# Optimization experiments

Measured on AMD Instinct MI355X. Metric: run time of the kernel, lower is better.

## Reference

```python
import jax, jax.numpy as jnp
import numpy as np

Z, DIM_IN, DIM_TS, DIM_OUT = 4096, 256, 2048, 256


def setup_inputs() -> dict:
    key = jax.random.key(0)
    k1, k2, k3 = jax.random.split(key, 3)
    features = jax.random.normal(k1, (Z, DIM_IN), dtype=jnp.float32)
    # Dense stand-in for the sparse CG buffer T: [dim_ts, dim_in * dim_in]
    T = jax.random.normal(k2, (DIM_TS, DIM_IN * DIM_IN), dtype=jnp.float32) * 0.02
    # KernelLinear output (learned mixing weights): [dim_out, dim_ts]
    W = jax.random.normal(k3, (DIM_OUT, DIM_TS), dtype=jnp.float32) * 0.02
    return {"features": features, "T": T, "W": W}


def reference(features, T, W):
    # features: [..., dim_in]; flatten leading dims as in the torch module
    *size, n = features.shape
    x = features.reshape(-1, n)                       # [z, i]
    # (T.t() @ W.T).T == W @ T ; reshape to [k, i, j]
    K = (W @ T).reshape(W.shape[0], n, n)             # [k, i, j]
    # per-sample bilinear (quadratic) form
    out = jnp.einsum('kij,zi,zj->zk', K, x, x)        # [z, k]
    return out.reshape(*size, -1)
```

## Files before the change

kernel.cpp:

```cpp
#include <hip/hip_runtime.h>

#define ZDIM 4096
#define DIN  256
#define DTS  2048
#define DOUT 256
#define CDIM 65536
#define SPLIT 16
#define NJS  8
#define NI   16
#define NST  (NJS * NI)
#define ZP   256
#define TILE_B 16384

typedef float fv4 __attribute__((ext_vector_type(4)));
typedef __bf16 bv8 __attribute__((ext_vector_type(8)));
typedef unsigned short u16;
typedef u16 uv8 __attribute__((ext_vector_type(8)));
typedef u16 uv4 __attribute__((ext_vector_type(4)));

union BC  { __bf16 b; u16 u; };
union VC8 { uv8 u; bv8 b; };
union FU  { unsigned u; float f; };

static __device__ __forceinline__ u16  f2b(float f){ BC c; c.b=(__bf16)f; return c.u; }
static __device__ __forceinline__ float bu(u16 v){ FU c; c.u = ((unsigned)v) << 16; return c.f; }
static __device__ __forceinline__ bv8  asb(uv8 x){ VC8 c; c.u=x; return c.b; }
static __device__ __forceinline__ uv8  pack8(fv4 a, fv4 b){
  uv8 p;
  p[0]=f2b(a[0]); p[1]=f2b(a[1]); p[2]=f2b(a[2]); p[3]=f2b(a[3]);
  p[4]=f2b(b[0]); p[5]=f2b(b[1]); p[6]=f2b(b[2]); p[7]=f2b(b[3]);
  return p;
}


__global__ __launch_bounds__(512, 2) void k_wt(const float* __restrict__ W,
                                               const float* __restrict__ T,
                                               u16* __restrict__ Km) {
  __shared__ u16 Al[256 * 40];
  __shared__ u16 Bl[32 * 128];
  const int tid  = threadIdx.x;
  const int lane = tid & 63;
  const int wave = tid >> 6;
  const int wk = (wave >> 1) * 64;
  const int wc = (wave & 1) * 64;
  const int cb = blockIdx.x * 128;
  const int ar = lane & 15, tg = lane >> 4;

  fv4 acc[4][4];
#pragma unroll
  for (int m = 0; m < 4; ++m)
#pragma unroll
    for (int n = 0; n < 4; ++n)
#pragma unroll
      for (int r = 0; r < 4; ++r) acc[m][n][r] = 0.f;

  for (int t0 = 0; t0 < DTS; t0 += 32) {
#pragma unroll
    for (int p = 0; p < 2; ++p) {
      int oct = tid + p * 512;
      int kr = oct >> 2, ts = (oct & 3) * 8;
      const float* src = W + (size_t)kr * DTS + t0 + ts;
      fv4 a = *(const fv4*)src, b = *(const fv4*)(src + 4);
      *(uv8*)&Al[kr * 40 + ts] = pack8(a, b);
    }
    {
      int tr = tid >> 4, co = (tid & 15) * 8;
      const float* src = T + (size_t)(t0 + tr) * CDIM + cb + co;
      fv4 a = *(const fv4*)src, b = *(const fv4*)(src + 4);
      *(uv8*)&Bl[tr * 128 + co] = pack8(a, b);
    }
    __syncthreads();
    bv8 af[4];
#pragma unroll
    for (int m = 0; m < 4; ++m)
      af[m] = asb(*(const uv8*)&Al[(wk + m * 16 + ar) * 40 + tg * 8]);
#pragma unroll
    for (int n = 0; n < 4; ++n) {
      uv8 bu2;
#pragma unroll
      for (int e = 0; e < 8; ++e)
        bu2[e] = Bl[(tg * 8 + e) * 128 + wc + n * 16 + ar];
      bv8 bf = asb(bu2);
#pragma unroll
      for (int m = 0; m < 4; ++m)
        acc[m][n] = __builtin_amdgcn_mfma_f32_16x16x32_bf16(af[m], bf, acc[m][n], 0, 0, 0);
    }
    __syncthreads();
  }
  const int ig = cb >> 8;
  const int j0 = cb & 255;
#pragma unroll
  for (int m = 0; m < 4; ++m)
#pragma unroll
    for (int n = 0; n < 4; ++n) {
      int j  = j0 + wc + n * 16;
      int js = j >> 5;
      int jj = j & 31;
      int sc = ig >> 4, il = ig & 15;
      size_t tb = ((size_t)(sc * 128 + js * 16 + il)) * TILE_B;
#pragma unroll
      for (int r = 0; r < 4; ++r) {
        int kr = wk + m * 16 + tg * 4 + r;
        int e  = kr * 64 + (jj + ar) * 2;
        e ^= ((e >> 7) & 7) << 4;
        *(u16*)((char*)Km + tb + e) = f2b(acc[m][n][r]);
      }
    }
}

__global__ __launch_bounds__(1024) void k_bil(const float* __restrict__ X,
                                              const u16* __restrict__ Km,
                                              u16* __restrict__ P) {
  __shared__ u16 Kl[2][TILE_B / 2];
  __shared__ u16 Xb[256 * 40];
  __shared__ u16 Xt[256 * 16];
  const int tid  = threadIdx.x;
  const int lane = tid & 63;
  const int wave = tid >> 6;
  const int wz   = (wave >> 2) * 64;
  const int wk   = (wave & 3) * 64;
  const int bid  = blockIdx.x;
  const int s    = bid & 15;
  const int z0   = (bid >> 4) * ZP;
  const int i0   = s * NI;
  const int ar   = lane & 15, tg = lane >> 4;

  const char* chunk = (const char*)Km + (size_t)s * NST * TILE_B;

  {
    int z = tid >> 2, ip = (tid & 3) * 4;
    fv4 v = *(const fv4*)&X[(size_t)(z0 + z) * DIN + i0 + ip];
    uv4 o;
#pragma unroll
    for (int e = 0; e < 4; ++e) o[e] = f2b(v[e]);
    *(uv4*)&Xt[z * 16 + ip] = o;
  }
  __builtin_amdgcn_global_load_lds(
      (const __attribute__((address_space(1))) void*)(chunk + (size_t)tid * 16),
      (__attribute__((address_space(3))) void*)((char*)&Kl[0][0] + tid * 16),
      16, 0, 0);

  int boff[4], aoff[4], xoff[4];
#pragma unroll
  for (int n = 0; n < 4; ++n) {
    int k = wk + n * 16 + ar;
    int e = k * 64 + tg * 16;
    boff[n] = e ^ (((e >> 7) & 7) << 4);
  }
#pragma unroll
  for (int m = 0; m < 4; ++m) {
    aoff[m] = (wz + m * 16 + ar) * 40 + tg * 8;
    xoff[m] = (wz + m * 16 + ar) * 16;
  }

  fv4 acc[4][4];
#pragma unroll
  for (int m = 0; m < 4; ++m)
#pragma unroll
    for (int n = 0; n < 4; ++n)
#pragma unroll
      for (int r = 0; r < 4; ++r) acc[m][n][r] = 0.f;

  for (int js = 0; js < NJS; ++js) {
    {
      int z = tid >> 2, seg = (tid & 3) * 8;
      const float* src = &X[(size_t)(z0 + z) * DIN + js * 32 + seg];
      fv4 a = *(const fv4*)src, b = *(const fv4*)(src + 4);
      *(uv8*)&Xb[z * 40 + seg] = pack8(a, b);
    }
    __syncthreads();

    uv8 af[4];
#pragma unroll
    for (int m = 0; m < 4; ++m)
      af[m] = *(const uv8*)&Xb[aoff[m]];

    for (int i = 0; i < NI; ++i) {
      const int st = js * NI + i;
      if (st + 1 < NST)
        __builtin_amdgcn_global_load_lds(
            (const __attribute__((address_space(1))) void*)(chunk + (size_t)(st + 1) * TILE_B + (size_t)tid * 16),
            (__attribute__((address_space(3))) void*)((char*)&Kl[(st + 1) & 1][0] + tid * 16),
            16, 0, 0);
      float xi[4];
#pragma unroll
      for (int m = 0; m < 4; ++m) xi[m] = bu(Xt[xoff[m] + i]);
      const char* kb = (const char*)&Kl[st & 1][0];
      bv8 bf[4];
#pragma unroll
      for (int n = 0; n < 4; ++n)
        bf[n] = asb(*(const uv8*)(kb + boff[n]));
#pragma unroll
      for (int m = 0; m < 4; ++m) {
        uv8 ap;
#pragma unroll
        for (int e = 0; e < 8; ++e) ap[e] = f2b(xi[m] * bu(af[m][e]));
        bv8 apb = asb(ap);
#pragma unroll
        for (int n = 0; n < 4; ++n)
          acc[m][n] = __builtin_amdgcn_mfma_f32_16x16x32_bf16(apb, bf[n], acc[m][n], 0, 0, 0);
      }
      __syncthreads();
    }
  }

  u16* dst = P + (size_t)s * (ZDIM * DOUT) + (size_t)z0 * DOUT;
#pragma unroll
  for (int m = 0; m < 4; ++m)
#pragma unroll
    for (int n = 0; n < 4; ++n)
#pragma unroll
      for (int r = 0; r < 4; ++r)
        dst[(size_t)(wz + m * 16 + tg * 4 + r) * DOUT + wk + n * 16 + ar] =
            f2b(acc[m][n][r]);
}

__global__ __launch_bounds__(256) void k_red(const u16* __restrict__ P,
                                             float* __restrict__ O) {
  size_t idx = ((size_t)blockIdx.x * 256 + threadIdx.x) * 4;
  fv4 acc;
#pragma unroll
  for (int r = 0; r < 4; ++r) acc[r] = 0.f;
#pragma unroll
  for (int p = 0; p < SPLIT; ++p) {
    uv4 v = *(const uv4*)&P[(size_t)p * (ZDIM * DOUT) + idx];
#pragma unroll
    for (int r = 0; r < 4; ++r) acc[r] += bu(v[r]);
  }
  *(fv4*)&O[idx] = acc;
}

extern "C" void kernel_launch(void* const* d_in, const int* in_sizes, int n_in,
                              void* d_out, int out_size, void* d_ws, size_t ws_size,
                              hipStream_t stream) {
  const float* feat = (const float*)d_in[0];
  const float* T    = (const float*)d_in[1];
  const float* W    = (const float*)d_in[2];
  float* out = (float*)d_out;

  u16* Km = (u16*)d_ws;
  u16* P  = (u16*)((char*)d_ws + (size_t)DOUT * CDIM * 2);

  k_wt <<<dim3(512),  dim3(512),  0, stream>>>(W, T, Km);
  k_bil<<<dim3(256),  dim3(1024), 0, stream>>>(feat, Km, P);
  k_red<<<dim3(1024), dim3(256),  0, stream>>>(P, out);
}
```

Measured before the change: 342.7 us.

## Triple-buffer K tiles and register-stage operands in both GEMM kernels

In k_bil, K tiles move from a double buffer to a triple buffer with a prefetch depth of two. The full __syncthreads is replaced by s_waitcnt vmcnt(1) plus a raw barrier, and the inner loop is unrolled with a macro. X operand fragments now load straight from global memory into registers instead of going through an LDS staging buffer, and the per-iteration xi scalars come from vectors preloaded once. In k_wt, W fragments load directly from global memory instead of LDS, T tiles are double-buffered with register prefetch and a padded stride, and the occupancy hint is raised to 4 blocks per SM. This aims to hide global-load latency and remove barriers and LDS traffic, but it adds redundant global W/X reads per wave and relies on hand-tuned vmcnt accounting that must match the order in which loads are issued.

```diff
diff --git a/kernel.cpp b/kernel.cpp
--- a/kernel.cpp
+++ b/kernel.cpp
@@ -33,11 +33,10 @@
 }
 
 
-__global__ __launch_bounds__(512, 2) void k_wt(const float* __restrict__ W,
+__global__ __launch_bounds__(512, 4) void k_wt(const float* __restrict__ W,
                                                const float* __restrict__ T,
                                                u16* __restrict__ Km) {
-  __shared__ u16 Al[256 * 40];
-  __shared__ u16 Bl[32 * 128];
+  __shared__ u16 Bl[2][32 * 130];
   const int tid  = threadIdx.x;
   const int lane = tid & 63;
   const int wave = tid >> 6;
@@ -45,6 +44,13 @@
   const int wc = (wave & 1) * 64;
   const int cb = blockIdx.x * 128;
   const int ar = lane & 15, tg = lane >> 4;
+  const int tr = tid >> 4, co = (tid & 15) * 8;
+
+  {
+    const float* src = T + (size_t)tr * CDIM + cb + co;
+    *(uv8*)&Bl[0][tr * 130 + co] = pack8(*(const fv4*)src, *(const fv4*)(src + 4));
+  }
+  __syncthreads();
 
   fv4 acc[4][4];
 #pragma unroll
@@ -54,38 +60,35 @@
 #pragma unroll
       for (int r = 0; r < 4; ++r) acc[m][n][r] = 0.f;
 
+  int buf = 0;
   for (int t0 = 0; t0 < DTS; t0 += 32) {
-#pragma unroll
-    for (int p = 0; p < 2; ++p) {
-      int oct = tid + p * 512;
-      int kr = oct >> 2, ts = (oct & 3) * 8;
-      const float* src = W + (size_t)kr * DTS + t0 + ts;
-      fv4 a = *(const fv4*)src, b = *(const fv4*)(src + 4);
-      *(uv8*)&Al[kr * 40 + ts] = pack8(a, b);
-    }
-    {
-      int tr = tid >> 4, co = (tid & 15) * 8;
-      const float* src = T + (size_t)(t0 + tr) * CDIM + cb + co;
-      fv4 a = *(const fv4*)src, b = *(const fv4*)(src + 4);
-      *(uv8*)&Bl[tr * 128 + co] = pack8(a, b);
-    }
-    __syncthreads();
+    const bool stg = (t0 + 32 < DTS);
+    fv4 ta, tb;
+    if (stg) {
+      const float* src = T + (size_t)(t0 + 32 + tr) * CDIM + cb + co;
+      ta = *(const fv4*)src; tb = *(const fv4*)(src + 4);
+    }
     bv8 af[4];
 #pragma unroll
-    for (int m = 0; m < 4; ++m)
-      af[m] = asb(*(const uv8*)&Al[(wk + m * 16 + ar) * 40 + tg * 8]);
+    for (int m = 0; m < 4; ++m) {
+      const float* wsrc = W + (size_t)(wk + m * 16 + ar) * DTS + t0 + tg * 8;
+      af[m] = asb(pack8(*(const fv4*)wsrc, *(const fv4*)(wsrc + 4)));
+    }
 #pragma unroll
     for (int n = 0; n < 4; ++n) {
       uv8 bu2;
 #pragma unroll
       for (int e = 0; e < 8; ++e)
-        bu2[e] = Bl[(tg * 8 + e) * 128 + wc + n * 16 + ar];
+        bu2[e] = Bl[buf][(tg * 8 + e) * 130 + wc + n * 16 + ar];
       bv8 bf = asb(bu2);
 #pragma unroll
       for (int m = 0; m < 4; ++m)
         acc[m][n] = __builtin_amdgcn_mfma_f32_16x16x32_bf16(af[m], bf, acc[m][n], 0, 0, 0);
     }
+    if (stg)
+      *(uv8*)&Bl[buf ^ 1][tr * 130 + co] = pack8(ta, tb);
     __syncthreads();
+    buf ^= 1;
   }
   const int ig = cb >> 8;
   const int j0 = cb & 255;
@@ -97,13 +100,13 @@
       int js = j >> 5;
       int jj = j & 31;
       int sc = ig >> 4, il = ig & 15;
-      size_t tb = ((size_t)(sc * 128 + js * 16 + il)) * TILE_B;
+      size_t tb2 = ((size_t)(sc * 128 + js * 16 + il)) * TILE_B;
 #pragma unroll
       for (int r = 0; r < 4; ++r) {
         int kr = wk + m * 16 + tg * 4 + r;
         int e  = kr * 64 + (jj + ar) * 2;
         e ^= ((e >> 7) & 7) << 4;
-        *(u16*)((char*)Km + tb + e) = f2b(acc[m][n][r]);
+        *(u16*)((char*)Km + tb2 + e) = f2b(acc[m][n][r]);
       }
     }
 }
@@ -111,8 +114,7 @@
 __global__ __launch_bounds__(1024) void k_bil(const float* __restrict__ X,
                                               const u16* __restrict__ Km,
                                               u16* __restrict__ P) {
-  __shared__ u16 Kl[2][TILE_B / 2];
-  __shared__ u16 Xb[256 * 40];
+  __shared__ u16 Kl[3][TILE_B / 2];
   __shared__ u16 Xt[256 * 16];
   const int tid  = threadIdx.x;
   const int lane = tid & 63;
@@ -137,10 +139,13 @@
   }
   __builtin_amdgcn_global_load_lds(
       (const __attribute__((address_space(1))) void*)(chunk + (size_t)tid * 16),
-      (__attribute__((address_space(3))) void*)((char*)&Kl[0][0] + tid * 16),
-      16, 0, 0);
-
-  int boff[4], aoff[4], xoff[4];
+      (__attribute__((address_space(3))) void*)((char*)&Kl[0][0] + tid * 16), 16, 0, 0);
+  __builtin_amdgcn_global_load_lds(
+      (const __attribute__((address_space(1))) void*)(chunk + TILE_B + (size_t)tid * 16),
+      (__attribute__((address_space(3))) void*)((char*)&Kl[1][0] + tid * 16), 16, 0, 0);
+  __syncthreads();
+
+  int boff[4], xoff[4];
 #pragma unroll
   for (int n = 0; n < 4; ++n) {
     int k = wk + n * 16 + ar;
@@ -148,9 +153,13 @@
     boff[n] = e ^ (((e >> 7) & 7) << 4);
   }
 #pragma unroll
+  for (int m = 0; m < 4; ++m) xoff[m] = (wz + m * 16 + ar) * 16;
+
+  uv8 xiv[4][2];
+#pragma unroll
   for (int m = 0; m < 4; ++m) {
-    aoff[m] = (wz + m * 16 + ar) * 40 + tg * 8;
-    xoff[m] = (wz + m * 16 + ar) * 16;
+    xiv[m][0] = *(const uv8*)&Xt[xoff[m]];
+    xiv[m][1] = *(const uv8*)&Xt[xoff[m] + 8];
   }
 
   fv4 acc[4][4];
@@ -161,48 +170,64 @@
 #pragma unroll
       for (int r = 0; r < 4; ++r) acc[m][n][r] = 0.f;
 
-  for (int js = 0; js < NJS; ++js) {
-    {
-      int z = tid >> 2, seg = (tid & 3) * 8;
-      const float* src = &X[(size_t)(z0 + z) * DIN + js * 32 + seg];
-      fv4 a = *(const fv4*)src, b = *(const fv4*)(src + 4);
-      *(uv8*)&Xb[z * 40 + seg] = pack8(a, b);
-    }
-    __syncthreads();
-
+  u16 *pa = &Kl[0][0], *pb = &Kl[1][0], *pc = &Kl[2][0];
+
+#define KB_ITER(ST, II, ISSUE, BARW)                                            \
+  {                                                                             \
+    if (ISSUE)                                                                  \
+      __builtin_amdgcn_global_load_lds(                                         \
+          (const __attribute__((address_space(1))) void*)(chunk +               \
+              (size_t)((ST) + 2) * TILE_B + (size_t)tid * 16),                  \
+          (__attribute__((address_space(3))) void*)((char*)pc + tid * 16),      \
+          16, 0, 0);                                                            \
+    bv8 bf_[4];                                                                 \
+    _Pragma("unroll")                                                           \
+    for (int n_ = 0; n_ < 4; ++n_)                                              \
+      bf_[n_] = asb(*(const uv8*)((const char*)pa + boff[n_]));                 \
+    _Pragma("unroll")                                                           \
+    for (int m_ = 0; m_ < 4; ++m_) {                                            \
+      float xi_ = bu(xiv[m_][(II) >> 3][(II) & 7]);                             \
+      uv8 ap_;                                                                  \
+      _Pragma("unroll")                                                         \
+      for (int e_ = 0; e_ < 8; ++e_) ap_[e_] = f2b(xi_ * bu(af[m_][e_]));       \
+      bv8 apb_ = asb(ap_);                                                      \
+      _Pragma("unroll")                                                         \
+      for (int n_ = 0; n_ < 4; ++n_)                                            \
+        acc[m_][n_] = __builtin_amdgcn_mfma_f32_16x16x32_bf16(                  \
+            apb_, bf_[n_], acc[m_][n_], 0, 0, 0);                               \
+    }                                                                           \
+    if ((BARW) >= 0) {                                                          \
+      if ((BARW) == 1) asm volatile("s_waitcnt vmcnt(1)" ::: "memory");         \
+      else             asm volatile("s_waitcnt vmcnt(0)" ::: "memory");         \
+      __builtin_amdgcn_s_barrier();                                             \
+      asm volatile("" ::: "memory");                                            \
+    }                                                                           \
+    u16* t_ = pa; pa = pb; pb = pc; pc = t_;                                    \
+  }
+
+  for (int js = 0; js < 7; ++js) {
     uv8 af[4];
 #pragma unroll
-    for (int m = 0; m < 4; ++m)
-      af[m] = *(const uv8*)&Xb[aoff[m]];
-
-    for (int i = 0; i < NI; ++i) {
-      const int st = js * NI + i;
-      if (st + 1 < NST)
-        __builtin_amdgcn_global_load_lds(
-            (const __attribute__((address_space(1))) void*)(chunk + (size_t)(st + 1) * TILE_B + (size_t)tid * 16),
-            (__attribute__((address_space(3))) void*)((char*)&Kl[(st + 1) & 1][0] + tid * 16),
-            16, 0, 0);
-      float xi[4];
-#pragma unroll
-      for (int m = 0; m < 4; ++m) xi[m] = bu(Xt[xoff[m] + i]);
-      const char* kb = (const char*)&Kl[st & 1][0];
-      bv8 bf[4];
-#pragma unroll
-      for (int n = 0; n < 4; ++n)
-        bf[n] = asb(*(const uv8*)(kb + boff[n]));
-#pragma unroll
-      for (int m = 0; m < 4; ++m) {
-        uv8 ap;
-#pragma unroll
-        for (int e = 0; e < 8; ++e) ap[e] = f2b(xi[m] * bu(af[m][e]));
-        bv8 apb = asb(ap);
-#pragma unroll
-        for (int n = 0; n < 4; ++n)
-          acc[m][n] = __builtin_amdgcn_mfma_f32_16x16x32_bf16(apb, bf[n], acc[m][n], 0, 0, 0);
-      }
-      __syncthreads();
-    }
-  }
+    for (int m = 0; m < 4; ++m) {
+      const float* row = X + (size_t)(z0 + wz + m * 16 + ar) * DIN + js * 32 + tg * 8;
+      af[m] = pack8(*(const fv4*)row, *(const fv4*)(row + 4));
+    }
+#pragma unroll
+    for (int i = 0; i < 16; ++i) KB_ITER(js * 16 + i, i, true, 1)
+  }
+  {
+    uv8 af[4];
+#pragma unroll
+    for (int m = 0; m < 4; ++m) {
+      const float* row = X + (size_t)(z0 + wz + m * 16 + ar) * DIN + 7 * 32 + tg * 8;
+      af[m] = pack8(*(const fv4*)row, *(const fv4*)(row + 4));
+    }
+#pragma unroll
+    for (int i = 0; i < 14; ++i) KB_ITER(112 + i, i, true, 1)
+    KB_ITER(126, 14, false, 0)
+    KB_ITER(127, 15, false, -1)
+  }
+#undef KB_ITER
 
   u16* dst = P + (size_t)s * (ZDIM * DOUT) + (size_t)z0 * DOUT;
 #pragma unroll
```

Result: slower. 1.076 ms (+213.9%).
